# Kernel tuning notes

Hardware: AMD Instinct MI355X
Metric: run time of the kernel (lower is better)

## Reference

```python
import jax, jax.numpy as jnp
import numpy as np

D_MODEL = 1024
NUM_HEADS = 16
D_K = D_MODEL // NUM_HEADS
B, N = 2, 2048


def setup_inputs() -> dict:
    key = jax.random.key(0)
    ks = jax.random.split(key, 11)
    s = 1.0 / np.sqrt(D_MODEL)
    inp = {
        "query": jax.random.normal(ks[0], (B, N, D_MODEL), jnp.float32),
        "key": jax.random.normal(ks[1], (B, N, D_MODEL), jnp.float32),
        "value": jax.random.normal(ks[2], (B, N, D_MODEL), jnp.float32),
        "w_q": jax.random.normal(ks[3], (D_MODEL, D_MODEL), jnp.float32) * s,
        "b_q": jax.random.normal(ks[4], (D_MODEL,), jnp.float32) * s,
        "w_k": jax.random.normal(ks[5], (D_MODEL, D_MODEL), jnp.float32) * s,
        "b_k": jax.random.normal(ks[6], (D_MODEL,), jnp.float32) * s,
        "w_v": jax.random.normal(ks[7], (D_MODEL, D_MODEL), jnp.float32) * s,
        "b_v": jax.random.normal(ks[8], (D_MODEL,), jnp.float32) * s,
        "w_o": jax.random.normal(ks[9], (D_MODEL, D_MODEL), jnp.float32) * s,
        "b_o": jax.random.normal(ks[10], (D_MODEL,), jnp.float32) * s,
    }
    return inp


def reference(query, key, value, w_q, b_q, w_k, b_k, w_v, b_v, w_o, b_o):
    Bq, Nq, _ = query.shape
    # projections (torch Linear: x @ W.T + b)
    Q = (query @ w_q.T + b_q).reshape(Bq, Nq, NUM_HEADS, D_K).transpose(0, 2, 1, 3)
    K = (key @ w_k.T + b_k).reshape(Bq, -1, NUM_HEADS, D_K).transpose(0, 2, 1, 3)
    V = (value @ w_v.T + b_v).reshape(Bq, -1, NUM_HEADS, D_K).transpose(0, 2, 1, 3)
    scores = jnp.einsum("bhqd,bhkd->bhqk", Q, K) / np.sqrt(D_K).astype(np.float32)
    attn = jax.nn.softmax(scores, axis=-1)  # dropout p=0.0 -> identity
    ctx = jnp.einsum("bhqk,bhkd->bhqd", attn, V)
    ctx = ctx.transpose(0, 2, 1, 3).reshape(Bq, Nq, D_MODEL)
    return ctx @ w_o.T + b_o
```

## Files before the change

kernel.cpp:

```cpp
#include <hip/hip_runtime.h>
#include <math.h>

#define D_MODEL 1024
#define NUM_HEADS 16
#define DK 64
#define BATCH 2
#define NSEQ 2048
#define MROWS (BATCH * NSEQ)

typedef __attribute__((ext_vector_type(8))) short bf16x8;
typedef __attribute__((ext_vector_type(4))) short s16x4;
typedef __attribute__((ext_vector_type(4))) float f32x4;
typedef unsigned short u16;

static __device__ __forceinline__ u16 f2bf_rne(float x) {
    union { float f; unsigned u; } v; v.f = x;
    unsigned r = v.u + 0x7fffu + ((v.u >> 16) & 1u);
    return (u16)(r >> 16);
}
static __device__ __forceinline__ void split_bf16(float x, u16& hi, u16& lo) {
    union { float f; unsigned u; } v; v.f = x;
    unsigned hb = v.u & 0xffff0000u;
    hi = (u16)(hb >> 16);
    union { unsigned u; float f; } hv; hv.u = hb;
    lo = f2bf_rne(x - hv.f);
}

#define AS1 __attribute__((address_space(1)))
#define AS3 __attribute__((address_space(3)))
static __device__ __forceinline__ void gl_lds16(const void* g, void* l) {
    __builtin_amdgcn_global_load_lds((AS1 void*)(uintptr_t)g, (AS3 void*)l, 16, 0, 0);
}

struct SplitN { const float* src[4]; u16* h[4]; u16* l[4]; };
__global__ __launch_bounds__(256)
void split_multi(SplitN args, int n8)
{
    const int w = blockIdx.y;
    const int i = blockIdx.x * 256 + threadIdx.x;
    if (i >= n8) return;
    const float* src = args.src[w];
    float4 a = ((const float4*)src)[2 * i];
    float4 b = ((const float4*)src)[2 * i + 1];
    float x[8] = {a.x, a.y, a.z, a.w, b.x, b.y, b.z, b.w};
    u16 hh[8], ll[8];
#pragma unroll
    for (int j = 0; j < 8; ++j) split_bf16(x[j], hh[j], ll[j]);
    *(uint4*)(args.h[w] + 8 * (size_t)i) = *(uint4*)hh;
    *(uint4*)(args.l[w] + 8 * (size_t)i) = *(uint4*)ll;
}

#define GBM 128
#define GBN 64
#define GBK 64

struct GemmDesc {
    const u16 *Ah, *Al, *Wh, *Wl;
    const float* bias;
    float* outF;
    u16 *outH, *outL;
    float scale;
    int mode;
};
struct GemmBatch { GemmDesc d[3]; };

__global__ __launch_bounds__(256)
void gemm_mfma_batch(GemmBatch batch, int M, int N, int K)
{
    __shared__ u16 SM[2 * GBM * GBK + 2 * GBN * GBK];
    u16* As_h = SM;
    u16* As_l = SM + GBM * GBK;
    u16* Ws_h = SM + 2 * GBM * GBK;
    u16* Ws_l = SM + 2 * GBM * GBK + GBN * GBK;

    const GemmDesc d = batch.d[blockIdx.z];
    const int tid  = threadIdx.x;
    const int wv   = tid >> 6, lane = tid & 63;
    const int quad = lane >> 4, lcol = lane & 15;
    const int bm = blockIdx.y * GBM, bn = blockIdx.x * GBN;
    const int wm = (wv >> 1) * 64, wn = (wv & 1) * 32;
    const int sj = lane >> 3, sg = lane & 7;
    const int sgx8 = ((sg ^ sj) << 3);

    f32x4 acc[4][2];
#pragma unroll
    for (int i = 0; i < 4; ++i)
#pragma unroll
        for (int j = 0; j < 2; ++j) acc[i][j] = (f32x4){0.f, 0.f, 0.f, 0.f};

    for (int k0 = 0; k0 < K; k0 += GBK) {
        __syncthreads();
#pragma unroll
        for (int c = 0; c < 4; ++c) {
            const int r0 = wv * 32 + c * 8;
            gl_lds16(d.Ah + (size_t)(bm + r0 + sj) * K + k0 + sgx8, As_h + r0 * GBK);
            gl_lds16(d.Al + (size_t)(bm + r0 + sj) * K + k0 + sgx8, As_l + r0 * GBK);
        }
#pragma unroll
        for (int c = 0; c < 2; ++c) {
            const int r0 = wv * 16 + c * 8;
            gl_lds16(d.Wh + (size_t)(bn + r0 + sj) * K + k0 + sgx8, Ws_h + r0 * GBK);
            gl_lds16(d.Wl + (size_t)(bn + r0 + sj) * K + k0 + sgx8, Ws_l + r0 * GBK);
        }
        __syncthreads();

#pragma unroll
        for (int hf = 0; hf < 2; ++hf) {
            const int sl = ((((hf << 2) + quad) ^ (lcol & 7)) << 3);
            bf16x8 bh[2], bl[2];
#pragma unroll
            for (int j = 0; j < 2; ++j) {
                const int rn = wn + (j << 4) + lcol;
                bh[j] = *(const bf16x8*)(Ws_h + rn * GBK + sl);
                bl[j] = *(const bf16x8*)(Ws_l + rn * GBK + sl);
            }
#pragma unroll
            for (int i = 0; i < 4; ++i) {
                const int rm = wm + (i << 4) + lcol;
                bf16x8 ah = *(const bf16x8*)(As_h + rm * GBK + sl);
                bf16x8 al = *(const bf16x8*)(As_l + rm * GBK + sl);
#pragma unroll
                for (int j = 0; j < 2; ++j) {
                    acc[i][j] = __builtin_amdgcn_mfma_f32_16x16x32_bf16(ah, bh[j], acc[i][j], 0, 0, 0);
                    acc[i][j] = __builtin_amdgcn_mfma_f32_16x16x32_bf16(al, bh[j], acc[i][j], 0, 0, 0);
                    acc[i][j] = __builtin_amdgcn_mfma_f32_16x16x32_bf16(ah, bl[j], acc[i][j], 0, 0, 0);
                }
            }
        }
    }

    if (d.mode == 2) {
        const int TS = 136;
        u16* T = SM;
        __syncthreads();
#pragma unroll
        for (int j = 0; j < 2; ++j) {
            const int cl = wn + (j << 4) + lcol;
            const float bj = d.bias[bn + cl];
#pragma unroll
            for (int i = 0; i < 4; ++i) {
                const int r0 = wm + (i << 4) + quad * 4;
                u16 pk[4];
#pragma unroll
                for (int r = 0; r < 4; ++r) pk[r] = f2bf_rne(acc[i][j][r] + bj);
                *(ushort4*)(T + cl * TS + r0) = *(ushort4*)pk;
            }
        }
        __syncthreads();
        const int dd = tid >> 2, pt = tid & 3;
        const int bidx = bm >> 11, hh = bn >> 6;
        u16* dst = d.outH + ((size_t)(bidx * NUM_HEADS + hh) * DK + dd) * NSEQ
                 + (bm & (NSEQ - 1)) + pt * 32;
        const u16* src = T + dd * TS + pt * 32;
#pragma unroll
        for (int k = 0; k < 4; ++k)
            ((uint4*)dst)[k] = *(const uint4*)(src + 8 * k);
        return;
    }

#pragma unroll
    for (int j = 0; j < 2; ++j) {
        const int col = bn + wn + (j << 4) + lcol;
        const float bj = d.bias[col];
#pragma unroll
        for (int i = 0; i < 4; ++i) {
#pragma unroll
            for (int r = 0; r < 4; ++r) {
                const int row = bm + wm + (i << 4) + quad * 4 + r;
                const float v = (acc[i][j][r] + bj) * d.scale;
                const size_t o = (size_t)row * N + col;
                if (d.mode == 0) {
                    d.outF[o] = v;
                } else {
                    u16 hi, lo;
                    split_bf16(v, hi, lo);
                    d.outH[o] = hi;
                    d.outL[o] = lo;
                }
            }
        }
    }
}

__global__ __launch_bounds__(256)
void flash_attn(const u16* __restrict__ Qh_g, const u16* __restrict__ Ql_g,
                const u16* __restrict__ Kh_g, const u16* __restrict__ Kl_g,
                const u16* __restrict__ Vt_g,
                u16* __restrict__ Ch_g, u16* __restrict__ Cl_g)
{
    __shared__ __align__(16) u16 Ks_h[64][72], Ks_l[64][72];
    __shared__ __align__(16) u16 Vs[64][72];

    const int tid  = threadIdx.x;
    const int wv   = tid >> 6;
    const int lane = tid & 63;
    const int quad = lane >> 4;
    const int lcol = lane & 15;
    const int q0   = blockIdx.x << 7;
    const int h    = blockIdx.y;
    const int b    = blockIdx.z;
    const size_t hbase  = (size_t)b * NSEQ * D_MODEL + (size_t)h * DK;
    const size_t vtbase = (size_t)(b * NUM_HEADS + h) * DK * NSEQ;

    bf16x8 bQh[2][2], bQl[2][2];
#pragma unroll
    for (int s = 0; s < 2; ++s) {
        const u16* qh = Qh_g + hbase + (size_t)(q0 + wv * 32 + s * 16 + lcol) * D_MODEL;
        const u16* ql = Ql_g + hbase + (size_t)(q0 + wv * 32 + s * 16 + lcol) * D_MODEL;
#pragma unroll
        for (int c = 0; c < 2; ++c) {
            bQh[s][c] = *(const bf16x8*)(qh + c * 32 + quad * 8);
            bQl[s][c] = *(const bf16x8*)(ql + c * 32 + quad * 8);
        }
    }

    f32x4 Oacc[2][4];
#pragma unroll
    for (int s = 0; s < 2; ++s)
#pragma unroll
        for (int t = 0; t < 4; ++t) Oacc[s][t] = (f32x4){0.f, 0.f, 0.f, 0.f};
    float mrow[2] = {-INFINITY, -INFINITY};
    float lrow[2] = {0.f, 0.f};

    const int lr = tid >> 2;
    const int lc = (tid & 3) << 4;

    for (int kt = 0; kt < NSEQ / 64; ++kt) {
        const int k0 = kt << 6;
        __syncthreads();
        {
            const u16* skh = Kh_g + hbase + (size_t)(k0 + lr) * D_MODEL + lc;
            const u16* skl = Kl_g + hbase + (size_t)(k0 + lr) * D_MODEL + lc;
            const u16* sv  = Vt_g + vtbase + (size_t)lr * NSEQ + k0 + lc;
            *(uint4*)&Ks_h[lr][lc]     = *(const uint4*)skh;
            *(uint4*)&Ks_h[lr][lc + 8] = *(const uint4*)(skh + 8);
            *(uint4*)&Ks_l[lr][lc]     = *(const uint4*)skl;
            *(uint4*)&Ks_l[lr][lc + 8] = *(const uint4*)(skl + 8);
            *(uint4*)&Vs[lr][lc]       = *(const uint4*)sv;
            *(uint4*)&Vs[lr][lc + 8]   = *(const uint4*)(sv + 8);
        }
        __syncthreads();

        f32x4 S[2][4];
#pragma unroll
        for (int t = 0; t < 4; ++t) {
            bf16x8 aKh0 = *(const bf16x8*)&Ks_h[(t << 4) + lcol][quad * 8];
            bf16x8 aKh1 = *(const bf16x8*)&Ks_h[(t << 4) + lcol][32 + quad * 8];
            bf16x8 aKl0 = *(const bf16x8*)&Ks_l[(t << 4) + lcol][quad * 8];
            bf16x8 aKl1 = *(const bf16x8*)&Ks_l[(t << 4) + lcol][32 + quad * 8];
#pragma unroll
            for (int s = 0; s < 2; ++s) {
                f32x4 a = (f32x4){0.f, 0.f, 0.f, 0.f};
                a = __builtin_amdgcn_mfma_f32_16x16x32_bf16(aKh0, bQh[s][0], a, 0, 0, 0);
                a = __builtin_amdgcn_mfma_f32_16x16x32_bf16(aKh1, bQh[s][1], a, 0, 0, 0);
                a = __builtin_amdgcn_mfma_f32_16x16x32_bf16(aKl0, bQh[s][0], a, 0, 0, 0);
                a = __builtin_amdgcn_mfma_f32_16x16x32_bf16(aKl1, bQh[s][1], a, 0, 0, 0);
                a = __builtin_amdgcn_mfma_f32_16x16x32_bf16(aKh0, bQl[s][0], a, 0, 0, 0);
                a = __builtin_amdgcn_mfma_f32_16x16x32_bf16(aKh1, bQl[s][1], a, 0, 0, 0);
                S[s][t] = a;
            }
        }

        bf16x8 pb[2][2];
#pragma unroll
        for (int s = 0; s < 2; ++s) {
            float m16 = -INFINITY;
#pragma unroll
            for (int t = 0; t < 4; ++t)
#pragma unroll
                for (int r = 0; r < 4; ++r) m16 = fmaxf(m16, S[s][t][r]);
            m16 = fmaxf(m16, __shfl_xor(m16, 16, 64));
            m16 = fmaxf(m16, __shfl_xor(m16, 32, 64));
            const float mn = fmaxf(mrow[s], m16);
            const float alpha = __expf(mrow[s] - mn);
            mrow[s] = mn;

            float p[4][4];
            float psum = 0.f;
#pragma unroll
            for (int t = 0; t < 4; ++t)
#pragma unroll
                for (int r = 0; r < 4; ++r) {
                    const float pv = __expf(S[s][t][r] - mn);
                    p[t][r] = pv;
                    psum += pv;
                }
            psum += __shfl_xor(psum, 16, 64);
            psum += __shfl_xor(psum, 32, 64);
            lrow[s] = alpha * lrow[s] + psum;

#pragma unroll
            for (int c = 0; c < 2; ++c) {
                bf16x8 v;
#pragma unroll
                for (int r = 0; r < 4; ++r) {
                    v[r]     = (short)f2bf_rne(p[2 * c][r]);
                    v[4 + r] = (short)f2bf_rne(p[2 * c + 1][r]);
                }
                pb[s][c] = v;
            }
#pragma unroll
            for (int t = 0; t < 4; ++t)
#pragma unroll
                for (int r = 0; r < 4; ++r) Oacc[s][t][r] *= alpha;
        }

#pragma unroll
        for (int dt = 0; dt < 4; ++dt) {
            const u16* vrow = &Vs[(dt << 4) + lcol][0];
#pragma unroll
            for (int c = 0; c < 2; ++c) {
                s16x4 alo = *(const s16x4*)(vrow + c * 32 + quad * 4);
                s16x4 ahi = *(const s16x4*)(vrow + c * 32 + 16 + quad * 4);
                bf16x8 aV;
#pragma unroll
                for (int r = 0; r < 4; ++r) { aV[r] = alo[r]; aV[4 + r] = ahi[r]; }
#pragma unroll
                for (int s = 0; s < 2; ++s)
                    Oacc[s][dt] = __builtin_amdgcn_mfma_f32_16x16x32_bf16(aV, pb[s][c], Oacc[s][dt], 0, 0, 0);
            }
        }
    }

#pragma unroll
    for (int s = 0; s < 2; ++s) {
        const float inv = 1.f / lrow[s];
        const size_t base = hbase + (size_t)(q0 + wv * 32 + s * 16 + lcol) * D_MODEL;
#pragma unroll
        for (int dt = 0; dt < 4; ++dt) {
            u16 hv[4], lv[4];
#pragma unroll
            for (int r = 0; r < 4; ++r)
                split_bf16(Oacc[s][dt][r] * inv, hv[r], lv[r]);
            const size_t o = base + (dt << 4) + quad * 4;
            *(ushort4*)(Ch_g + o) = *(ushort4*)hv;
            *(ushort4*)(Cl_g + o) = *(ushort4*)lv;
        }
    }
}

extern "C" void kernel_launch(void* const* d_in, const int* in_sizes, int n_in,
                              void* d_out, int out_size, void* d_ws, size_t ws_size,
                              hipStream_t stream)
{
    const float* query = (const float*)d_in[0];
    const float* key_i = (const float*)d_in[1];
    const float* value = (const float*)d_in[2];
    const float* w_q   = (const float*)d_in[3];
    const float* b_q   = (const float*)d_in[4];
    const float* w_k   = (const float*)d_in[5];
    const float* b_k   = (const float*)d_in[6];
    const float* w_v   = (const float*)d_in[7];
    const float* b_v   = (const float*)d_in[8];
    const float* w_o   = (const float*)d_in[9];
    const float* b_o   = (const float*)d_in[10];
    float* out = (float*)d_out;

    const size_t WE = (size_t)D_MODEL * D_MODEL;
    const size_t AE = (size_t)MROWS * D_MODEL;

    u16* p = (u16*)d_ws;
    u16* Wqh = p;            u16* Wql = Wqh + WE;
    u16* Wkh = Wql + WE;     u16* Wkl = Wkh + WE;
    u16* Wvh = Wkl + WE;     u16* Wvl = Wvh + WE;
    u16* Woh = Wvl + WE;     u16* Wol = Woh + WE;
    u16* base = Wol + WE;

    SplitN ws4;
    ws4.src[0] = w_q; ws4.h[0] = Wqh; ws4.l[0] = Wql;
    ws4.src[1] = w_k; ws4.h[1] = Wkh; ws4.l[1] = Wkl;
    ws4.src[2] = w_v; ws4.h[2] = Wvh; ws4.l[2] = Wvl;
    ws4.src[3] = w_o; ws4.h[3] = Woh; ws4.l[3] = Wol;
    split_multi<<<dim3((unsigned)(WE / 8 / 256), 4), 256, 0, stream>>>(ws4, (int)(WE / 8));

    const float qscale = 0.125f;
    dim3 fgrid(NSEQ / 128, NUM_HEADS, BATCH);
    dim3 ggrid1(D_MODEL / GBN, MROWS / GBM, 1);
    const int an8 = (int)(AE / 8);

    const size_t fused_bytes = 2 * (8 * WE + 11 * AE);
    if (ws_size >= fused_bytes) {
        u16* INqh = base;          u16* INql = INqh + AE;
        u16* INkh = INql + AE;     u16* INkl = INkh + AE;
        u16* INvh = INkl + AE;     u16* INvl = INvh + AE;
        u16* Qph  = INvl + AE;     u16* Qpl  = Qph + AE;
        u16* Kph  = Qpl + AE;      u16* Kpl  = Kph + AE;
        u16* VT   = Kpl + AE;
        u16* Ch   = INqh;          u16* Cl   = INql;

        SplitN as3;
        as3.src[0] = query; as3.h[0] = INqh; as3.l[0] = INql;
        as3.src[1] = key_i; as3.h[1] = INkh; as3.l[1] = INkl;
        as3.src[2] = value; as3.h[2] = INvh; as3.l[2] = INvl;
        as3.src[3] = query; as3.h[3] = INqh; as3.l[3] = INql;
        split_multi<<<dim3((unsigned)(AE / 8 / 256), 3), 256, 0, stream>>>(as3, an8);

        GemmBatch gb;
        gb.d[0] = {INqh, INql, Wqh, Wql, b_q, nullptr, Qph, Qpl, qscale, 1};
        gb.d[1] = {INkh, INkl, Wkh, Wkl, b_k, nullptr, Kph, Kpl, 1.0f,   1};
        gb.d[2] = {INvh, INvl, Wvh, Wvl, b_v, nullptr, VT,  nullptr, 1.0f, 2};
        dim3 ggrid3(D_MODEL / GBN, MROWS / GBM, 3);
        gemm_mfma_batch<<<ggrid3, 256, 0, stream>>>(gb, MROWS, D_MODEL, D_MODEL);

        flash_attn<<<fgrid, 256, 0, stream>>>(Qph, Qpl, Kph, Kpl, VT, Ch, Cl);

        GemmBatch go;
        go.d[0] = {Ch, Cl, Woh, Wol, b_o, out, nullptr, nullptr, 1.0f, 0};
        gemm_mfma_batch<<<ggrid1, 256, 0, stream>>>(go, MROWS, D_MODEL, D_MODEL);
    } else {
        u16* INh = base;           u16* INl = INh + AE;
        u16* Qph = INl + AE;       u16* Qpl = Qph + AE;
        u16* Kph = Qpl + AE;       u16* Kpl = Kph + AE;
        u16* VT  = Kpl + AE;
        u16* Ch  = INh;            u16* Cl  = INl;

        SplitN s1;
        s1.src[0] = query; s1.h[0] = INh; s1.l[0] = INl;
        s1.src[1] = s1.src[2] = s1.src[3] = query;
        s1.h[1] = s1.h[2] = s1.h[3] = INh; s1.l[1] = s1.l[2] = s1.l[3] = INl;

        GemmBatch g;
        s1.src[0] = query;
        split_multi<<<dim3((unsigned)(AE / 8 / 256), 1), 256, 0, stream>>>(s1, an8);
        g.d[0] = {INh, INl, Wqh, Wql, b_q, nullptr, Qph, Qpl, qscale, 1};
        gemm_mfma_batch<<<ggrid1, 256, 0, stream>>>(g, MROWS, D_MODEL, D_MODEL);

        s1.src[0] = key_i;
        split_multi<<<dim3((unsigned)(AE / 8 / 256), 1), 256, 0, stream>>>(s1, an8);
        g.d[0] = {INh, INl, Wkh, Wkl, b_k, nullptr, Kph, Kpl, 1.0f, 1};
        gemm_mfma_batch<<<ggrid1, 256, 0, stream>>>(g, MROWS, D_MODEL, D_MODEL);

        s1.src[0] = value;
        split_multi<<<dim3((unsigned)(AE / 8 / 256), 1), 256, 0, stream>>>(s1, an8);
        g.d[0] = {INh, INl, Wvh, Wvl, b_v, nullptr, VT, nullptr, 1.0f, 2};
        gemm_mfma_batch<<<ggrid1, 256, 0, stream>>>(g, MROWS, D_MODEL, D_MODEL);

        flash_attn<<<fgrid, 256, 0, stream>>>(Qph, Qpl, Kph, Kpl, VT, Ch, Cl);

        g.d[0] = {Ch, Cl, Woh, Wol, b_o, out, nullptr, nullptr, 1.0f, 0};
        gemm_mfma_batch<<<ggrid1, 256, 0, stream>>>(g, MROWS, D_MODEL, D_MODEL);
    }
}
```

Measured before the change: 339.2 us.

## Retile split-bf16 GEMMs to 128-wide N tiles and use async LDS loads in attention

The projection GEMM is rewritten as a templated kernel with 128-column N tiles, K step 32, and MT-configurable M tiles (128 rows for QKV, 64 rows for the output projection). This raises per-wave MFMA work per LDS fragment load and changes the XOR swizzle. The V-transpose epilogue now runs in two passes, one per head. Flash attention switches K/V tile staging from register round-trip stores to direct global-to-LDS loads with an XOR swizzle in place of row padding. The halved K step means more barriers per tile, and the larger accumulator set raises register pressure and may reduce occupancy.

```diff
diff --git a/kernel.cpp b/kernel.cpp
--- a/kernel.cpp
+++ b/kernel.cpp
@@ -50,10 +50,6 @@
     *(uint4*)(args.l[w] + 8 * (size_t)i) = *(uint4*)ll;
 }
 
-#define GBM 128
-#define GBN 64
-#define GBK 64
-
 struct GemmDesc {
     const u16 *Ah, *Al, *Wh, *Wl;
     const float* bias;
@@ -64,106 +60,113 @@
 };
 struct GemmBatch { GemmDesc d[3]; };
 
+template<int MT>
 __global__ __launch_bounds__(256)
-void gemm_mfma_batch(GemmBatch batch, int M, int N, int K)
+void gemm_mfma_v2(GemmBatch batch, int M, int N, int K)
 {
-    __shared__ u16 SM[2 * GBM * GBK + 2 * GBN * GBK];
+    constexpr int BM = MT * 32;
+    __shared__ u16 SM[(2 * BM + 2 * 128) * 32];
     u16* As_h = SM;
-    u16* As_l = SM + GBM * GBK;
-    u16* Ws_h = SM + 2 * GBM * GBK;
-    u16* Ws_l = SM + 2 * GBM * GBK + GBN * GBK;
+    u16* As_l = As_h + BM * 32;
+    u16* Ws_h = As_l + BM * 32;
+    u16* Ws_l = Ws_h + 128 * 32;
 
     const GemmDesc d = batch.d[blockIdx.z];
     const int tid  = threadIdx.x;
     const int wv   = tid >> 6, lane = tid & 63;
     const int quad = lane >> 4, lcol = lane & 15;
-    const int bm = blockIdx.y * GBM, bn = blockIdx.x * GBN;
-    const int wm = (wv >> 1) * 64, wn = (wv & 1) * 32;
-    const int sj = lane >> 3, sg = lane & 7;
-    const int sgx8 = ((sg ^ sj) << 3);
-
-    f32x4 acc[4][2];
-#pragma unroll
-    for (int i = 0; i < 4; ++i)
-#pragma unroll
-        for (int j = 0; j < 2; ++j) acc[i][j] = (f32x4){0.f, 0.f, 0.f, 0.f};
-
-    for (int k0 = 0; k0 < K; k0 += GBK) {
+    const int bm = blockIdx.y * BM, bn = blockIdx.x * 128;
+    const int wm = (wv >> 1) * (MT * 16), wn = (wv & 1) * 64;
+    const int srow = lane >> 2;
+    const int g4o  = (((lane & 3) ^ (srow & 3)) << 3);
+    const int xk   = (lcol & 3);
+
+    f32x4 acc[MT][4];
+#pragma unroll
+    for (int i = 0; i < MT; ++i)
+#pragma unroll
+        for (int j = 0; j < 4; ++j) acc[i][j] = (f32x4){0.f, 0.f, 0.f, 0.f};
+
+    constexpr int AIPW = BM / 64;
+
+    for (int k0 = 0; k0 < K; k0 += 32) {
         __syncthreads();
 #pragma unroll
-        for (int c = 0; c < 4; ++c) {
-            const int r0 = wv * 32 + c * 8;
-            gl_lds16(d.Ah + (size_t)(bm + r0 + sj) * K + k0 + sgx8, As_h + r0 * GBK);
-            gl_lds16(d.Al + (size_t)(bm + r0 + sj) * K + k0 + sgx8, As_l + r0 * GBK);
+        for (int c = 0; c < AIPW; ++c) {
+            const int rb = (wv * AIPW + c) * 16;
+            gl_lds16(d.Ah + (size_t)(bm + rb + srow) * K + k0 + g4o, As_h + rb * 32);
+            gl_lds16(d.Al + (size_t)(bm + rb + srow) * K + k0 + g4o, As_l + rb * 32);
         }
 #pragma unroll
         for (int c = 0; c < 2; ++c) {
-            const int r0 = wv * 16 + c * 8;
-            gl_lds16(d.Wh + (size_t)(bn + r0 + sj) * K + k0 + sgx8, Ws_h + r0 * GBK);
-            gl_lds16(d.Wl + (size_t)(bn + r0 + sj) * K + k0 + sgx8, Ws_l + r0 * GBK);
+            const int rb = (wv * 2 + c) * 16;
+            gl_lds16(d.Wh + (size_t)(bn + rb + srow) * K + k0 + g4o, Ws_h + rb * 32);
+            gl_lds16(d.Wl + (size_t)(bn + rb + srow) * K + k0 + g4o, Ws_l + rb * 32);
         }
         __syncthreads();
 
-#pragma unroll
-        for (int hf = 0; hf < 2; ++hf) {
-            const int sl = ((((hf << 2) + quad) ^ (lcol & 7)) << 3);
-            bf16x8 bh[2], bl[2];
-#pragma unroll
-            for (int j = 0; j < 2; ++j) {
-                const int rn = wn + (j << 4) + lcol;
-                bh[j] = *(const bf16x8*)(Ws_h + rn * GBK + sl);
-                bl[j] = *(const bf16x8*)(Ws_l + rn * GBK + sl);
-            }
-#pragma unroll
-            for (int i = 0; i < 4; ++i) {
-                const int rm = wm + (i << 4) + lcol;
-                bf16x8 ah = *(const bf16x8*)(As_h + rm * GBK + sl);
-                bf16x8 al = *(const bf16x8*)(As_l + rm * GBK + sl);
-#pragma unroll
-                for (int j = 0; j < 2; ++j) {
-                    acc[i][j] = __builtin_amdgcn_mfma_f32_16x16x32_bf16(ah, bh[j], acc[i][j], 0, 0, 0);
-                    acc[i][j] = __builtin_amdgcn_mfma_f32_16x16x32_bf16(al, bh[j], acc[i][j], 0, 0, 0);
-                    acc[i][j] = __builtin_amdgcn_mfma_f32_16x16x32_bf16(ah, bl[j], acc[i][j], 0, 0, 0);
+        bf16x8 bh[4], bl[4];
+#pragma unroll
+        for (int j = 0; j < 4; ++j) {
+            const int off = (wn + (j << 4) + lcol) * 32 + ((quad ^ xk) << 3);
+            bh[j] = *(const bf16x8*)(Ws_h + off);
+            bl[j] = *(const bf16x8*)(Ws_l + off);
+        }
+#pragma unroll
+        for (int i = 0; i < MT; ++i) {
+            const int off = (wm + (i << 4) + lcol) * 32 + ((quad ^ xk) << 3);
+            bf16x8 ah = *(const bf16x8*)(As_h + off);
+            bf16x8 al = *(const bf16x8*)(As_l + off);
+#pragma unroll
+            for (int j = 0; j < 4; ++j) {
+                acc[i][j] = __builtin_amdgcn_mfma_f32_16x16x32_bf16(ah, bh[j], acc[i][j], 0, 0, 0);
+                acc[i][j] = __builtin_amdgcn_mfma_f32_16x16x32_bf16(al, bh[j], acc[i][j], 0, 0, 0);
+                acc[i][j] = __builtin_amdgcn_mfma_f32_16x16x32_bf16(ah, bl[j], acc[i][j], 0, 0, 0);
+            }
+        }
+    }
+
+    if constexpr (MT == 4) {
+        if (batch.d[blockIdx.z].mode == 2) {
+            u16* T = SM;
+#pragma unroll
+            for (int p = 0; p < 2; ++p) {
+                __syncthreads();
+                if ((wv & 1) == p) {
+#pragma unroll
+                    for (int j = 0; j < 4; ++j) {
+                        const int cl = (j << 4) + lcol;
+                        const float bj = d.bias[bn + wn + (j << 4) + lcol];
+#pragma unroll
+                        for (int i = 0; i < 4; ++i) {
+                            u16 pk[4];
+#pragma unroll
+                            for (int r = 0; r < 4; ++r)
+                                pk[r] = f2bf_rne(acc[i][j][r] + bj);
+                            *(ushort4*)(T + cl * 136 + wm + (i << 4) + quad * 4) = *(ushort4*)pk;
+                        }
+                    }
                 }
-            }
-        }
-    }
-
-    if (d.mode == 2) {
-        const int TS = 136;
-        u16* T = SM;
-        __syncthreads();
-#pragma unroll
-        for (int j = 0; j < 2; ++j) {
-            const int cl = wn + (j << 4) + lcol;
-            const float bj = d.bias[bn + cl];
-#pragma unroll
-            for (int i = 0; i < 4; ++i) {
-                const int r0 = wm + (i << 4) + quad * 4;
-                u16 pk[4];
-#pragma unroll
-                for (int r = 0; r < 4; ++r) pk[r] = f2bf_rne(acc[i][j][r] + bj);
-                *(ushort4*)(T + cl * TS + r0) = *(ushort4*)pk;
-            }
-        }
-        __syncthreads();
-        const int dd = tid >> 2, pt = tid & 3;
-        const int bidx = bm >> 11, hh = bn >> 6;
-        u16* dst = d.outH + ((size_t)(bidx * NUM_HEADS + hh) * DK + dd) * NSEQ
-                 + (bm & (NSEQ - 1)) + pt * 32;
-        const u16* src = T + dd * TS + pt * 32;
-#pragma unroll
-        for (int k = 0; k < 4; ++k)
-            ((uint4*)dst)[k] = *(const uint4*)(src + 8 * k);
-        return;
-    }
-
-#pragma unroll
-    for (int j = 0; j < 2; ++j) {
+                __syncthreads();
+                const int dd = tid >> 2, nt = tid & 3;
+                u16* dst = d.outH
+                    + ((size_t)((bm >> 11) * NUM_HEADS + (bn >> 6) + p) * DK + dd) * NSEQ
+                    + (bm & (NSEQ - 1)) + nt * 32;
+                const u16* srcT = T + dd * 136 + nt * 32;
+#pragma unroll
+                for (int k = 0; k < 4; ++k)
+                    ((uint4*)dst)[k] = *(const uint4*)(srcT + 8 * k);
+            }
+            return;
+        }
+    }
+
+#pragma unroll
+    for (int j = 0; j < 4; ++j) {
         const int col = bn + wn + (j << 4) + lcol;
         const float bj = d.bias[col];
 #pragma unroll
-        for (int i = 0; i < 4; ++i) {
+        for (int i = 0; i < MT; ++i) {
 #pragma unroll
             for (int r = 0; r < 4; ++r) {
                 const int row = bm + wm + (i << 4) + quad * 4 + r;
@@ -188,8 +191,7 @@
                 const u16* __restrict__ Vt_g,
                 u16* __restrict__ Ch_g, u16* __restrict__ Cl_g)
 {
-    __shared__ __align__(16) u16 Ks_h[64][72], Ks_l[64][72];
-    __shared__ __align__(16) u16 Vs[64][72];
+    __shared__ __align__(16) u16 Ks_h[64 * 64], Ks_l[64 * 64], Vs[64 * 64];
 
     const int tid  = threadIdx.x;
     const int wv   = tid >> 6;
@@ -222,32 +224,33 @@
     float mrow[2] = {-INFINITY, -INFINITY};
     float lrow[2] = {0.f, 0.f};
 
-    const int lr = tid >> 2;
-    const int lc = (tid & 3) << 4;
+    const int srow8 = lane >> 3;
+    const int g8o   = (((lane & 7) ^ srow8) << 3);
+    const int xk    = (lcol & 7);
 
     for (int kt = 0; kt < NSEQ / 64; ++kt) {
         const int k0 = kt << 6;
         __syncthreads();
-        {
-            const u16* skh = Kh_g + hbase + (size_t)(k0 + lr) * D_MODEL + lc;
-            const u16* skl = Kl_g + hbase + (size_t)(k0 + lr) * D_MODEL + lc;
-            const u16* sv  = Vt_g + vtbase + (size_t)lr * NSEQ + k0 + lc;
-            *(uint4*)&Ks_h[lr][lc]     = *(const uint4*)skh;
-            *(uint4*)&Ks_h[lr][lc + 8] = *(const uint4*)(skh + 8);
-            *(uint4*)&Ks_l[lr][lc]     = *(const uint4*)skl;
-            *(uint4*)&Ks_l[lr][lc + 8] = *(const uint4*)(skl + 8);
-            *(uint4*)&Vs[lr][lc]       = *(const uint4*)sv;
-            *(uint4*)&Vs[lr][lc + 8]   = *(const uint4*)(sv + 8);
+#pragma unroll
+        for (int c = 0; c < 2; ++c) {
+            const int rb = wv * 16 + c * 8;
+            gl_lds16(Kh_g + hbase + (size_t)(k0 + rb + srow8) * D_MODEL + g8o, Ks_h + rb * 64);
+            gl_lds16(Kl_g + hbase + (size_t)(k0 + rb + srow8) * D_MODEL + g8o, Ks_l + rb * 64);
+            gl_lds16(Vt_g + vtbase + (size_t)(rb + srow8) * NSEQ + k0 + g8o, Vs + rb * 64);
         }
         __syncthreads();
 
         f32x4 S[2][4];
 #pragma unroll
         for (int t = 0; t < 4; ++t) {
-            bf16x8 aKh0 = *(const bf16x8*)&Ks_h[(t << 4) + lcol][quad * 8];
-            bf16x8 aKh1 = *(const bf16x8*)&Ks_h[(t << 4) + lcol][32 + quad * 8];
-            bf16x8 aKl0 = *(const bf16x8*)&Ks_l[(t << 4) + lcol][quad * 8];
-            bf16x8 aKl1 = *(const bf16x8*)&Ks_l[(t << 4) + lcol][32 + quad * 8];
+            const u16* krh = Ks_h + ((t << 4) + lcol) * 64;
+            const u16* krl = Ks_l + ((t << 4) + lcol) * 64;
+            const int s0 = ((quad ^ xk) << 3);
+            const int s1 = (((4 + quad) ^ xk) << 3);
+            bf16x8 aKh0 = *(const bf16x8*)(krh + s0);
+            bf16x8 aKh1 = *(const bf16x8*)(krh + s1);
+            bf16x8 aKl0 = *(const bf16x8*)(krl + s0);
+            bf16x8 aKl1 = *(const bf16x8*)(krl + s1);
 #pragma unroll
             for (int s = 0; s < 2; ++s) {
                 f32x4 a = (f32x4){0.f, 0.f, 0.f, 0.f};
@@ -307,11 +310,12 @@
 
 #pragma unroll
         for (int dt = 0; dt < 4; ++dt) {
-            const u16* vrow = &Vs[(dt << 4) + lcol][0];
+            const u16* vr = Vs + ((dt << 4) + lcol) * 64;
 #pragma unroll
             for (int c = 0; c < 2; ++c) {
-                s16x4 alo = *(const s16x4*)(vrow + c * 32 + quad * 4);
-                s16x4 ahi = *(const s16x4*)(vrow + c * 32 + 16 + quad * 4);
+                const int s0 = (((c * 4 + (quad >> 1)) ^ xk) << 3) + ((quad & 1) << 2);
+                s16x4 alo = *(const s16x4*)(vr + s0);
+                s16x4 ahi = *(const s16x4*)(vr + (s0 ^ 16));
                 bf16x8 aV;
 #pragma unroll
                 for (int r = 0; r < 4; ++r) { aV[r] = alo[r]; aV[4 + r] = ahi[r]; }
@@ -375,7 +379,9 @@
 
     const float qscale = 0.125f;
     dim3 fgrid(NSEQ / 128, NUM_HEADS, BATCH);
-    dim3 ggrid1(D_MODEL / GBN, MROWS / GBM, 1);
+    dim3 qkvgrid(D_MODEL / 128, MROWS / 128, 3);
+    dim3 outgrid(D_MODEL / 128, MROWS / 64, 1);
+    dim3 qkvgrid1(D_MODEL / 128, MROWS / 128, 1);
     const int an8 = (int)(AE / 8);
 
     const size_t fused_bytes = 2 * (8 * WE + 11 * AE);
@@ -399,14 +405,13 @@
         gb.d[0] = {INqh, INql, Wqh, Wql, b_q, nullptr, Qph, Qpl, qscale, 1};
         gb.d[1] = {INkh, INkl, Wkh, Wkl, b_k, nullptr, Kph, Kpl, 1.0f,   1};
         gb.d[2] = {INvh, INvl, Wvh, Wvl, b_v, nullptr, VT,  nullptr, 1.0f, 2};
-        dim3 ggrid3(D_MODEL / GBN, MROWS / GBM, 3);
-        gemm_mfma_batch<<<ggrid3, 256, 0, stream>>>(gb, MROWS, D_MODEL, D_MODEL);
+        gemm_mfma_v2<4><<<qkvgrid, 256, 0, stream>>>(gb, MROWS, D_MODEL, D_MODEL);
 
         flash_attn<<<fgrid, 256, 0, stream>>>(Qph, Qpl, Kph, Kpl, VT, Ch, Cl);
 
         GemmBatch go;
         go.d[0] = {Ch, Cl, Woh, Wol, b_o, out, nullptr, nullptr, 1.0f, 0};
-        gemm_mfma_batch<<<ggrid1, 256, 0, stream>>>(go, MROWS, D_MODEL, D_MODEL);
+        gemm_mfma_v2<2><<<outgrid, 256, 0, stream>>>(go, MROWS, D_MODEL, D_MODEL);
     } else {
         u16* INh = base;           u16* INl = INh + AE;
         u16* Qph = INl + AE;       u16* Qpl = Qph + AE;
@@ -423,21 +428,21 @@
         s1.src[0] = query;
         split_multi<<<dim3((unsigned)(AE / 8 / 256), 1), 256, 0, stream>>>(s1, an8);
         g.d[0] = {INh, INl, Wqh, Wql, b_q, nullptr, Qph, Qpl, qscale, 1};
-        gemm_mfma_batch<<<ggrid1, 256, 0, stream>>>(g, MROWS, D_MODEL, D_MODEL);
+        gemm_mfma_v2<4><<<qkvgrid1, 256, 0, stream>>>(g, MROWS, D_MODEL, D_MODEL);
 
         s1.src[0] = key_i;
         split_multi<<<dim3((unsigned)(AE / 8 / 256), 1), 256, 0, stream>>>(s1, an8);
         g.d[0] = {INh, INl, Wkh, Wkl, b_k, nullptr, Kph, Kpl, 1.0f, 1};
-        gemm_mfma_batch<<<ggrid1, 256, 0, stream>>>(g, MROWS, D_MODEL, D_MODEL);
+        gemm_mfma_v2<4><<<qkvgrid1, 256, 0, stream>>>(g, MROWS, D_MODEL, D_MODEL);
 
         s1.src[0] = value;
         split_multi<<<dim3((unsigned)(AE / 8 / 256), 1), 256, 0, stream>>>(s1, an8);
         g.d[0] = {INh, INl, Wvh, Wvl, b_v, nullptr, VT, nullptr, 1.0f, 2};
-        gemm_mfma_batch<<<ggrid1, 256, 0, stream>>>(g, MROWS, D_MODEL, D_MODEL);
+        gemm_mfma_v2<4><<<qkvgrid1, 256, 0, stream>>>(g, MROWS, D_MODEL, D_MODEL);
 
         flash_attn<<<fgrid, 256, 0, stream>>>(Qph, Qpl, Kph, Kpl, VT, Ch, Cl);
 
         g.d[0] = {Ch, Cl, Woh, Wol, b_o, out, nullptr, nullptr, 1.0f, 0};
-        gemm_mfma_batch<<<ggrid1, 256, 0, stream>>>(g, MROWS, D_MODEL, D_MODEL);
-    }
-}
+        gemm_mfma_v2<2><<<outgrid, 256, 0, stream>>>(g, MROWS, D_MODEL, D_MODEL);
+    }
+}
```

New measurement: 365.6 us. 7.8% more time.
